# Kernel optimization log

Measured on AMD Instinct MI355X. Metric: run time of the kernel, lower is better.

The kernel has to match this reference:

```python
import jax, jax.numpy as jnp
import numpy as np

B = 65536

def setup_inputs() -> dict:
    key = jax.random.key(0)
    ks = jax.random.split(key, 6)
    x = jax.random.normal(ks[0], (B, 784), dtype=jnp.float32)
    w_conv = jnp.ones((3, 3), dtype=jnp.float32)  # Parameter(ones((3,3)))
    w1 = jax.random.normal(ks[1], (676, 256), dtype=jnp.float32) * 0.04
    b1 = jax.random.normal(ks[2], (256,), dtype=jnp.float32) * 0.01
    w2 = jax.random.normal(ks[3], (256, 10), dtype=jnp.float32) * 0.06
    b2 = jax.random.normal(ks[4], (10,), dtype=jnp.float32) * 0.01
    return {"x": x, "w_conv": w_conv, "w1": w1, "b1": b1, "w2": w2, "b2": b2}

def reference(x, w_conv, w1, b1, w2, b2):
    b = x.shape[0]
    img = x.reshape(b, 1, 28, 28)
    # Convolve() is cross-correlation (no kernel flip), 'VALID': 28->26
    kern = w_conv.reshape(1, 1, 3, 3)
    conv = jax.lax.conv_general_dilated(
        img, kern, window_strides=(1, 1), padding='VALID',
        dimension_numbers=('NCHW', 'OIHW', 'NCHW'))  # (B,1,26,26)
    feat = conv.reshape(b, 676)
    h = jax.nn.relu(feat @ w1 + b1)  # (B,256)
    return h @ w2 + b2               # (B,10)
```

## Files before the change

### kernel.cpp

```cpp
#include <hip/hip_runtime.h>
#include <hip/hip_bf16.h>
#include <stdint.h>

typedef __bf16 bf16;
typedef __attribute__((ext_vector_type(8))) __bf16 bf16x8;
typedef __attribute__((ext_vector_type(4))) float f32x4;

#define KREAL 784
#define KPAD  800

__global__ __launch_bounds__(256) void prep_w1t(const float* __restrict__ w_conv,
                                                const float* __restrict__ w1,
                                                bf16* __restrict__ W1t) {
    const int k = blockIdx.x;
    const int n = threadIdx.x;
    float s = 0.0f;
    if (k < KREAL) {
        const int r = k / 28, c = k % 28;
        #pragma unroll
        for (int di = 0; di < 3; ++di) {
            const int i = r - di;
            if (i < 0 || i >= 26) continue;
            #pragma unroll
            for (int dj = 0; dj < 3; ++dj) {
                const int j = c - dj;
                if (j < 0 || j >= 26) continue;
                s += w_conv[di * 3 + dj] * w1[(i * 26 + j) * 256 + n];
            }
        }
    }
    W1t[n * KPAD + k] = (bf16)s;
}

__global__ __launch_bounds__(256, 2) void fused_mlp(
    const float* __restrict__ x,
    const bf16*  __restrict__ W1t,
    const float* __restrict__ b1,
    const float* __restrict__ w2,
    const float* __restrict__ b2,
    float* __restrict__ out)
{
    __shared__ bf16  As[128][32];
    __shared__ bf16  Bs[256][32];
    __shared__ float w2s[256][10];
    __shared__ float b1s[256];
    __shared__ float b2s[10];

    const int t    = threadIdx.x;
    const int wave = t >> 6;
    const int lane = t & 63;
    const int c    = lane & 15;
    const int q    = lane >> 4;

    const int row0 = blockIdx.x * 128;

    for (int i = t; i < 2560; i += 256) ((float*)w2s)[i] = w2[i];
    b1s[t] = b1[t];
    if (t < 10) b2s[t] = b2[t];

    const int arow  = t >> 1;
    const int ahalf = t & 1;
    const float* xsrc = x + (size_t)(row0 + arow) * KREAL + ahalf * 16;
    const bf16* bsrc = W1t + t * KPAD;

    f32x4 acc[2][16];
    #pragma unroll
    for (int mt = 0; mt < 2; ++mt)
        #pragma unroll
        for (int nt = 0; nt < 16; ++nt)
            acc[mt][nt] = (f32x4){0.f, 0.f, 0.f, 0.f};

    #pragma unroll 1
    for (int k0 = 0; k0 < KPAD; k0 += 32) {
        float4 av0, av1, av2, av3;
        const bool valid = (k0 + ahalf * 16) < KREAL;
        const float4* a4 = (const float4*)(xsrc + k0);
        if (valid) { av0 = a4[0]; av1 = a4[1]; av2 = a4[2]; av3 = a4[3]; }
        else       { av0 = av1 = av2 = av3 = (float4){0.f, 0.f, 0.f, 0.f}; }
        const uint4* b4 = (const uint4*)(bsrc + k0);
        uint4 bv0 = b4[0], bv1 = b4[1], bv2 = b4[2], bv3 = b4[3];

        __syncthreads();

        bf16x8 p0, p1;
        p0[0] = (bf16)av0.x; p0[1] = (bf16)av0.y; p0[2] = (bf16)av0.z; p0[3] = (bf16)av0.w;
        p0[4] = (bf16)av1.x; p0[5] = (bf16)av1.y; p0[6] = (bf16)av1.z; p0[7] = (bf16)av1.w;
        p1[0] = (bf16)av2.x; p1[1] = (bf16)av2.y; p1[2] = (bf16)av2.z; p1[3] = (bf16)av2.w;
        p1[4] = (bf16)av3.x; p1[5] = (bf16)av3.y; p1[6] = (bf16)av3.z; p1[7] = (bf16)av3.w;
        *(bf16x8*)&As[arow][ahalf * 16]     = p0;
        *(bf16x8*)&As[arow][ahalf * 16 + 8] = p1;
        *(uint4*)&Bs[t][0]  = bv0;
        *(uint4*)&Bs[t][8]  = bv1;
        *(uint4*)&Bs[t][16] = bv2;
        *(uint4*)&Bs[t][24] = bv3;

        __syncthreads();

        bf16x8 a0 = *(const bf16x8*)&As[wave * 32 +      c][q * 8];
        bf16x8 a1 = *(const bf16x8*)&As[wave * 32 + 16 + c][q * 8];
        #pragma unroll
        for (int nt = 0; nt < 16; ++nt) {
            bf16x8 b = *(const bf16x8*)&Bs[nt * 16 + c][q * 8];
            acc[0][nt] = __builtin_amdgcn_mfma_f32_16x16x32_bf16(a0, b, acc[0][nt], 0, 0, 0);
            acc[1][nt] = __builtin_amdgcn_mfma_f32_16x16x32_bf16(a1, b, acc[1][nt], 0, 0, 0);
        }
    }

    float bl[16];
    #pragma unroll
    for (int nt = 0; nt < 16; ++nt) bl[nt] = b1s[nt * 16 + c];

    #pragma unroll
    for (int mt = 0; mt < 2; ++mt)
        #pragma unroll
        for (int nt = 0; nt < 16; ++nt)
            #pragma unroll
            for (int r = 0; r < 4; ++r) {
                float v = acc[mt][nt][r] + bl[nt];
                acc[mt][nt][r] = v > 0.f ? v : 0.f;
            }

    #pragma unroll 1
    for (int j = 0; j < 10; ++j) {
        float wj[16];
        #pragma unroll
        for (int nt = 0; nt < 16; ++nt) wj[nt] = w2s[nt * 16 + c][j];
        const float b2j = b2s[j];
        #pragma unroll
        for (int mt = 0; mt < 2; ++mt)
            #pragma unroll
            for (int r = 0; r < 4; ++r) {
                float s = 0.f;
                #pragma unroll
                for (int nt = 0; nt < 16; ++nt) s += acc[mt][nt][r] * wj[nt];
                s += __shfl_xor(s, 1, 64);
                s += __shfl_xor(s, 2, 64);
                s += __shfl_xor(s, 4, 64);
                s += __shfl_xor(s, 8, 64);
                if (c == j) {
                    const int row = row0 + wave * 32 + mt * 16 + q * 4 + r;
                    out[(size_t)row * 10 + j] = s + b2j;
                }
            }
    }
}

extern "C" void kernel_launch(void* const* d_in, const int* in_sizes, int n_in,
                              void* d_out, int out_size, void* d_ws, size_t ws_size,
                              hipStream_t stream) {
    const float* x  = (const float*)d_in[0];
    const float* wc = (const float*)d_in[1];
    const float* w1 = (const float*)d_in[2];
    const float* b1 = (const float*)d_in[3];
    const float* w2 = (const float*)d_in[4];
    const float* b2 = (const float*)d_in[5];
    float* out = (float*)d_out;
    bf16* W1t = (bf16*)d_ws;

    prep_w1t<<<dim3(KPAD), dim3(256), 0, stream>>>(wc, w1, W1t);
    fused_mlp<<<dim3(65536 / 128), dim3(256), 0, stream>>>(x, W1t, b1, w2, b2, out);
}
```

Baseline: 325.4 us.

## Load A fragments directly to registers and stream B via global_load_lds

Drops the A shared-memory tile: each lane now reads its own x elements from global memory straight into MFMA fragment registers and converts them to bf16. The W1t tile is copied into LDS with the global_load_lds direct-to-LDS builtin instead of staging through registers. The aim is to cut LDS traffic, register staging and VGPR pressure. In exchange, the per-lane x reads are less coalesced (32-byte chunks spread across rows), and the LDS write layout must match the prior Bs[256][32] indexing.

```diff
diff --git a/kernel.cpp b/kernel.cpp
--- a/kernel.cpp
+++ b/kernel.cpp
@@ -8,6 +8,9 @@
 
 #define KREAL 784
 #define KPAD  800
+
+#define GLOBAL_AS __attribute__((address_space(1)))
+#define LDS_AS    __attribute__((address_space(3)))
 
 __global__ __launch_bounds__(256) void prep_w1t(const float* __restrict__ w_conv,
                                                 const float* __restrict__ w1,
@@ -40,7 +43,6 @@
     const float* __restrict__ b2,
     float* __restrict__ out)
 {
-    __shared__ bf16  As[128][32];
     __shared__ bf16  Bs[256][32];
     __shared__ float w2s[256][10];
     __shared__ float b1s[256];
@@ -58,10 +60,11 @@
     b1s[t] = b1[t];
     if (t < 10) b2s[t] = b2[t];
 
-    const int arow  = t >> 1;
-    const int ahalf = t & 1;
-    const float* xsrc = x + (size_t)(row0 + arow) * KREAL + ahalf * 16;
-    const bf16* bsrc = W1t + t * KPAD;
+    const float* arow0 = x + (size_t)(row0 + wave * 32 + c) * KREAL + q * 8;
+    const float* arow1 = arow0 + (size_t)16 * KREAL;
+
+    const bf16* bsrc0 = W1t + (size_t)(wave * 64 + (lane >> 2)) * KPAD + (lane & 3) * 8;
+    char* bdst0 = (char*)(&Bs[0][0]) + wave * 4096;
 
     f32x4 acc[2][16];
     #pragma unroll
@@ -72,32 +75,32 @@
 
     #pragma unroll 1
     for (int k0 = 0; k0 < KPAD; k0 += 32) {
-        float4 av0, av1, av2, av3;
-        const bool valid = (k0 + ahalf * 16) < KREAL;
-        const float4* a4 = (const float4*)(xsrc + k0);
-        if (valid) { av0 = a4[0]; av1 = a4[1]; av2 = a4[2]; av3 = a4[3]; }
-        else       { av0 = av1 = av2 = av3 = (float4){0.f, 0.f, 0.f, 0.f}; }
-        const uint4* b4 = (const uint4*)(bsrc + k0);
-        uint4 bv0 = b4[0], bv1 = b4[1], bv2 = b4[2], bv3 = b4[3];
+        __syncthreads();
+
+        #pragma unroll
+        for (int j = 0; j < 4; ++j) {
+            __builtin_amdgcn_global_load_lds(
+                (const GLOBAL_AS void*)(bsrc0 + k0 + j * 16 * KPAD),
+                (LDS_AS void*)(bdst0 + j * 1024), 16, 0, 0);
+        }
+
+        float4 f0a, f0b, f1a, f1b;
+        if (k0 + q * 8 < KREAL) {
+            const float* p0 = arow0 + k0;
+            const float* p1 = arow1 + k0;
+            f0a = *(const float4*)p0; f0b = *(const float4*)(p0 + 4);
+            f1a = *(const float4*)p1; f1b = *(const float4*)(p1 + 4);
+        } else {
+            f0a = f0b = f1a = f1b = (float4){0.f, 0.f, 0.f, 0.f};
+        }
+        bf16x8 a0, a1;
+        a0[0] = (bf16)f0a.x; a0[1] = (bf16)f0a.y; a0[2] = (bf16)f0a.z; a0[3] = (bf16)f0a.w;
+        a0[4] = (bf16)f0b.x; a0[5] = (bf16)f0b.y; a0[6] = (bf16)f0b.z; a0[7] = (bf16)f0b.w;
+        a1[0] = (bf16)f1a.x; a1[1] = (bf16)f1a.y; a1[2] = (bf16)f1a.z; a1[3] = (bf16)f1a.w;
+        a1[4] = (bf16)f1b.x; a1[5] = (bf16)f1b.y; a1[6] = (bf16)f1b.z; a1[7] = (bf16)f1b.w;
 
         __syncthreads();
 
-        bf16x8 p0, p1;
-        p0[0] = (bf16)av0.x; p0[1] = (bf16)av0.y; p0[2] = (bf16)av0.z; p0[3] = (bf16)av0.w;
-        p0[4] = (bf16)av1.x; p0[5] = (bf16)av1.y; p0[6] = (bf16)av1.z; p0[7] = (bf16)av1.w;
-        p1[0] = (bf16)av2.x; p1[1] = (bf16)av2.y; p1[2] = (bf16)av2.z; p1[3] = (bf16)av2.w;
-        p1[4] = (bf16)av3.x; p1[5] = (bf16)av3.y; p1[6] = (bf16)av3.z; p1[7] = (bf16)av3.w;
-        *(bf16x8*)&As[arow][ahalf * 16]     = p0;
-        *(bf16x8*)&As[arow][ahalf * 16 + 8] = p1;
-        *(uint4*)&Bs[t][0]  = bv0;
-        *(uint4*)&Bs[t][8]  = bv1;
-        *(uint4*)&Bs[t][16] = bv2;
-        *(uint4*)&Bs[t][24] = bv3;
-
-        __syncthreads();
-
-        bf16x8 a0 = *(const bf16x8*)&As[wave * 32 +      c][q * 8];
-        bf16x8 a1 = *(const bf16x8*)&As[wave * 32 + 16 + c][q * 8];
         #pragma unroll
         for (int nt = 0; nt < 16; ++nt) {
             bf16x8 b = *(const bf16x8*)&Bs[nt * 16 + c][q * 8];
```

After: 317.9 us. -2.3%, faster.
